# Kernel optimization log

Measured on AMD Instinct MI355X. Metric: run time of the kernel, lower is better.

Reference implementation:

```python
import jax, jax.numpy as jnp
import numpy as np

K = 128
T_X = 4
DATA_LENGTH = 512
B_GROUPS = 64
B = B_GROUPS * DATA_LENGTH
INV_SQRT2 = 0.7071067811865476  # 1/sqrt(2), haar reconstruction filter coeff


def setup_inputs() -> dict:
    key = jax.random.key(0)
    ks = jax.random.split(key, 9)
    x = jax.random.normal(ks[0], (B, T_X, K), jnp.float32)
    y = jax.random.normal(ks[1], (B, 1, K), jnp.float32)
    s = 1.0 / np.sqrt(K).astype(np.float32)
    Wq = jax.random.normal(ks[2], (K, K), jnp.float32) * s
    Wk = jax.random.normal(ks[3], (K, K), jnp.float32) * s
    Wv = jax.random.normal(ks[4], (K, K), jnp.float32) * s
    conv_w = jax.random.normal(ks[5], (K, 2 * K), jnp.float32) * (1.0 / np.sqrt(2 * K).astype(np.float32))
    conv_b = jax.random.normal(ks[6], (K,), jnp.float32) * 0.01
    bn_gamma = jnp.ones((K,), jnp.float32)
    bn_beta = jnp.zeros((K,), jnp.float32)
    bn_mean = jax.random.normal(ks[7], (K,), jnp.float32) * 0.1
    bn_var = jax.random.uniform(ks[8], (K,), jnp.float32, 0.5, 1.5)
    return dict(x=x, y=y, Wq=Wq, Wk=Wk, Wv=Wv, conv_w=conv_w, conv_b=conv_b,
                bn_gamma=bn_gamma, bn_beta=bn_beta, bn_mean=bn_mean, bn_var=bn_var,
                data_length=DATA_LENGTH)


def _idwt_haar(L, H):
    # inverse 1D haar transform along last dim: (Bg, C, 1, T) -> (Bg, C, 1, 2T)
    even = (L + H) * INV_SQRT2
    odd = (L - H) * INV_SQRT2
    out = jnp.stack([even, odd], axis=-1)  # (..., T, 2)
    return out.reshape(L.shape[:-1] + (L.shape[-1] * 2,))


def reference(x, y, Wq, Wk, Wv, conv_w, conv_b, bn_gamma, bn_beta, bn_mean, bn_var, data_length):
    b, t_x, k = x.shape  # t_x = 4 bands, heads = 1, t_y = 1
    q = jnp.einsum('btk,ok->bto', y, Wq)                      # (b, 1, k)
    keys = jnp.einsum('bsk,ok->bso', x, Wk) * (1.0 / (k ** 0.5))  # (b, 4, k)
    v = jnp.einsum('bsk,ok->bso', x, Wv)                      # (b, 4, k)
    dot = jnp.einsum('bto,bso->bs', q, keys)                  # (b, 4)
    w = jax.nn.softmax(dot, axis=1)                           # softmax over the 4 bands
    outs = w[:, :, None] * v                                  # (b, 4, k) band-weighted values
    Bg = b // data_length
    # per band: (b, k) -> (Bg, dl, 1, k) -> permute -> (Bg, k, 1, dl)
    o = outs.reshape(Bg, data_length, t_x, k).transpose(2, 0, 3, 1)  # (4, Bg, k, dl)
    o = o[:, :, :, None, :]                                   # (4, Bg, k, 1, dl)
    out_L = _idwt_haar(o[0], o[1])                            # (Bg, k, 1, 2*dl)
    out_H = _idwt_haar(o[2], o[3])
    out = jnp.concatenate([out_L, out_H], axis=1)             # (Bg, 2k, 1, 2*dl)
    # transition: 1x1 conv + BN (eval mode) + LeakyReLU(0.01)
    z = jnp.einsum('bcij,oc->boij', out, conv_w) + conv_b[None, :, None, None]
    scale = (bn_gamma * jax.lax.rsqrt(bn_var + 1e-5))[None, :, None, None]
    z = (z - bn_mean[None, :, None, None]) * scale + bn_beta[None, :, None, None]
    return jnp.where(z > 0, z, 0.01 * z)
```

## Files before the change

### kernel.cpp

```cpp
#include <hip/hip_runtime.h>
#include <stdint.h>

typedef __attribute__((ext_vector_type(8))) short bf16x8;
typedef __attribute__((ext_vector_type(4))) float f32x4;

__device__ __forceinline__ unsigned short f2bf(float x) {
    union { float f; uint32_t u; } v; v.f = x;
    uint32_t r = v.u + 0x7FFFu + ((v.u >> 16) & 1u);
    return (unsigned short)(r >> 16);
}
__device__ __forceinline__ uint32_t pack2bf(float a, float b) {
    return (uint32_t)f2bf(a) | ((uint32_t)f2bf(b) << 16);
}
__device__ __forceinline__ float bf2f(uint32_t lo) {
    union { uint32_t u; float f; } v; v.u = lo << 16; return v.f;
}
__device__ __forceinline__ float lrelu(float v) { return v > 0.f ? v : 0.01f * v; }

__global__ __launch_bounds__(256) void precompute_kernel(
    const float* __restrict__ Wq, const float* __restrict__ Wk,
    const float* __restrict__ Wv, const float* __restrict__ conv_w,
    const float* __restrict__ conv_b, const float* __restrict__ bn_gamma,
    const float* __restrict__ bn_beta, const float* __restrict__ bn_mean,
    const float* __restrict__ bn_var,
    unsigned short* __restrict__ Gh, unsigned short* __restrict__ Gl,
    unsigned short* __restrict__ Mh,
    float* __restrict__ scale2, float* __restrict__ bias2)
{
    __shared__ float lds0[2176];
    __shared__ float lds1[2176];
    const int tid = threadIdx.x;
    const int bid = blockIdx.x;

    if (bid == 192) {
        if (tid < 128) {
            float sc = bn_gamma[tid] * rsqrtf(bn_var[tid] + 1e-5f);
            scale2[tid] = sc;
            bias2[tid]  = (conv_b[tid] - bn_mean[tid]) * sc + bn_beta[tid];
        }
        return;
    }

    if (bid < 64) {
        int i0 = (bid >> 3) << 4, j0 = (bid & 7) << 4;
        #pragma unroll
        for (int t = 0; t < 8; ++t) {
            int e = tid + t * 256;
            int o = e >> 4, c = e & 15;
            lds0[o * 17 + c] = Wk[o * 128 + i0 + c];
            lds1[o * 17 + c] = Wq[o * 128 + j0 + c];
        }
        __syncthreads();
        int ti = tid >> 4, tj = tid & 15;
        float sum = 0.f;
        #pragma unroll 8
        for (int o = 0; o < 128; ++o) sum += lds0[o * 17 + ti] * lds1[o * 17 + tj];
        float val = sum * 0.08838834764831845f;
        unsigned short h = f2bf(val);
        int idx = (i0 + ti) * 128 + j0 + tj;
        Gh[idx] = h;
        Gl[idx] = f2bf(val - bf2f(h));
    } else {
        int rel = bid - 64;
        int o0 = (rel >> 4) << 4, c0 = (rel & 15) << 4;
        int cw0 = (c0 >> 7) << 7, cc0 = c0 & 127;
        #pragma unroll
        for (int t = 0; t < 8; ++t) {
            int e = tid + t * 256;
            int to = e >> 7, k = e & 127;
            lds0[to * 132 + k] = conv_w[(o0 + to) * 256 + cw0 + k];
            int kk = e >> 4, c = e & 15;
            lds1[kk * 17 + c] = Wv[kk * 128 + cc0 + c];
        }
        __syncthreads();
        int to = tid >> 4, tc = tid & 15;
        float sum = 0.f;
        #pragma unroll 8
        for (int k = 0; k < 128; ++k) sum += lds0[to * 132 + k] * lds1[k * 17 + tc];
        Mh[(o0 + to) * 256 + c0 + tc] = f2bf(sum * 0.7071067811865476f);
    }
}

#define AADDR(row, gi)   (((row) << 8) + ((((gi) ^ ((row) & 7))) << 4))

__global__ __launch_bounds__(256, 4) void fused_kernel(
    const float* __restrict__ x, const float* __restrict__ y,
    const unsigned short* __restrict__ Gh, const unsigned short* __restrict__ Gl,
    const unsigned short* __restrict__ Mh,
    const float* __restrict__ scale2, const float* __restrict__ bias2,
    float* __restrict__ out)
{
    __shared__ __align__(16) unsigned char smem[32768];
    float* gbufF = (float*)(smem + 16384);

    const int tid = threadIdx.x;
    const int w = tid >> 6;
    const int l = tid & 63;
    const int quad = l >> 4;
    const int i16 = l & 15;
    const int bid = blockIdx.x;
    const int b0 = bid * 32;

    union F8 { float4 v[2]; float f[8]; };
    F8 X[2][4];
    #pragma unroll
    for (int pass = 0; pass < 2; ++pass) {
        int b_loc = 8 * w + pass * 4 + quad;
        const float* xb = x + (size_t)(b0 + b_loc) * 512 + i16 * 8;
        #pragma unroll
        for (int t = 0; t < 4; ++t) {
            X[pass][t].v[0] = *(const float4*)(xb + t * 128);
            X[pass][t].v[1] = *(const float4*)(xb + t * 128 + 4);
        }
    }
    const int ks0 = bid & 3;
    bf16x8 pgh[2], pgl[2];
    #pragma unroll
    for (int n = 0; n < 2; ++n) {
        int off = ((2 * w + n) * 16 + i16) * 128 + ks0 * 32 + quad * 8;
        pgh[n] = *(const bf16x8*)(Gh + off);
        pgl[n] = *(const bf16x8*)(Gl + off);
    }

    {
        const float* yb = y + (size_t)b0 * 128;
        #pragma unroll
        for (int it = 0; it < 2; ++it) {
            int j = tid + it * 256;
            int row = j >> 4, gk = j & 15;
            float4 v0 = *(const float4*)(yb + row * 128 + gk * 8);
            float4 v1 = *(const float4*)(yb + row * 128 + gk * 8 + 4);
            float f[8] = {v0.x, v0.y, v0.z, v0.w, v1.x, v1.y, v1.z, v1.w};
            uint32_t hi[4], lo[4];
            #pragma unroll
            for (int e = 0; e < 4; ++e) {
                unsigned short h0 = f2bf(f[2 * e]), h1 = f2bf(f[2 * e + 1]);
                hi[e] = (uint32_t)h0 | ((uint32_t)h1 << 16);
                lo[e] = (uint32_t)f2bf(f[2 * e] - bf2f(h0)) |
                        ((uint32_t)f2bf(f[2 * e + 1] - bf2f(h1)) << 16);
            }
            int addr = AADDR(row, gk);
            *(uint4*)(smem + addr)        = make_uint4(hi[0], hi[1], hi[2], hi[3]);
            *(uint4*)(smem + 8192 + addr) = make_uint4(lo[0], lo[1], lo[2], lo[3]);
        }
    }
    __syncthreads();

    {
        f32x4 accg[2][2];
        #pragma unroll
        for (int rt = 0; rt < 2; ++rt)
            #pragma unroll
            for (int n = 0; n < 2; ++n) accg[rt][n] = (f32x4){0.f, 0.f, 0.f, 0.f};
        #pragma unroll
        for (int ks = 0; ks < 4; ++ks) {
            int ksr = (ks + bid) & 3;
            bf16x8 ah[2], al[2];
            #pragma unroll
            for (int rt = 0; rt < 2; ++rt) {
                int row = 16 * rt + i16;
                int addr = AADDR(row, ksr * 4 + quad);
                ah[rt] = *(const bf16x8*)(smem + addr);
                al[rt] = *(const bf16x8*)(smem + 8192 + addr);
            }
            #pragma unroll
            for (int n = 0; n < 2; ++n) {
                bf16x8 bh, bl;
                if (ks == 0) { bh = pgh[n]; bl = pgl[n]; }
                else {
                    int off = ((2 * w + n) * 16 + i16) * 128 + ksr * 32 + quad * 8;
                    bh = *(const bf16x8*)(Gh + off);
                    bl = *(const bf16x8*)(Gl + off);
                }
                #pragma unroll
                for (int rt = 0; rt < 2; ++rt) {
                    accg[rt][n] = __builtin_amdgcn_mfma_f32_16x16x32_bf16(ah[rt], bh, accg[rt][n], 0, 0, 0);
                    accg[rt][n] = __builtin_amdgcn_mfma_f32_16x16x32_bf16(al[rt], bh, accg[rt][n], 0, 0, 0);
                    accg[rt][n] = __builtin_amdgcn_mfma_f32_16x16x32_bf16(ah[rt], bl, accg[rt][n], 0, 0, 0);
                }
            }
        }
        #pragma unroll
        for (int n = 0; n < 2; ++n) {
            int i = (2 * w + n) * 16 + i16;
            #pragma unroll
            for (int rt = 0; rt < 2; ++rt)
                #pragma unroll
                for (int r = 0; r < 4; ++r)
                    gbufF[(16 * rt + quad * 4 + r) * 128 + i] = accg[rt][n][r];
        }
    }
    __syncthreads();

    #pragma unroll
    for (int pass = 0; pass < 2; ++pass) {
        int b_loc = 8 * w + pass * 4 + quad;
        float4 ga = *(const float4*)(gbufF + b_loc * 128 + i16 * 8);
        float4 gb = *(const float4*)(gbufF + b_loc * 128 + i16 * 8 + 4);
        float p[4];
        #pragma unroll
        for (int t = 0; t < 4; ++t) {
            float4 a = X[pass][t].v[0], b = X[pass][t].v[1];
            p[t] = a.x * ga.x + a.y * ga.y + a.z * ga.z + a.w * ga.w
                 + b.x * gb.x + b.y * gb.y + b.z * gb.z + b.w * gb.w;
        }
        #pragma unroll
        for (int off = 8; off >= 1; off >>= 1) {
            p[0] += __shfl_xor(p[0], off);
            p[1] += __shfl_xor(p[1], off);
            p[2] += __shfl_xor(p[2], off);
            p[3] += __shfl_xor(p[3], off);
        }
        float mx = fmaxf(fmaxf(p[0], p[1]), fmaxf(p[2], p[3]));
        float e0 = __expf(p[0] - mx), e1 = __expf(p[1] - mx);
        float e2 = __expf(p[2] - mx), e3 = __expf(p[3] - mx);
        float inv = 1.f / (e0 + e1 + e2 + e3);
        float w0 = e0 * inv, w1 = e1 * inv, w2 = e2 * inv, w3 = e3 * inv;
        int r0 = 2 * b_loc, r1 = r0 + 1;
        int a0 = AADDR(r0, i16), a1 = AADDR(r1, i16);
        uint32_t eL[4], oL[4], eH[4], oH[4];
        #pragma unroll
        for (int e = 0; e < 4; ++e) {
            int c0 = 2 * e, c1 = 2 * e + 1;
            eL[e] = pack2bf(w0 * X[pass][0].f[c0] + w1 * X[pass][1].f[c0], w0 * X[pass][0].f[c1] + w1 * X[pass][1].f[c1]);
            oL[e] = pack2bf(w0 * X[pass][0].f[c0] - w1 * X[pass][1].f[c0], w0 * X[pass][0].f[c1] - w1 * X[pass][1].f[c1]);
            eH[e] = pack2bf(w2 * X[pass][2].f[c0] + w3 * X[pass][3].f[c0], w2 * X[pass][2].f[c1] + w3 * X[pass][3].f[c1]);
            oH[e] = pack2bf(w2 * X[pass][2].f[c0] - w3 * X[pass][3].f[c0], w2 * X[pass][2].f[c1] - w3 * X[pass][3].f[c1]);
        }
        *(uint4*)(smem + a0)         = make_uint4(eL[0], eL[1], eL[2], eL[3]);
        *(uint4*)(smem + a1)         = make_uint4(oL[0], oL[1], oL[2], oL[3]);
        *(uint4*)(smem + 16384 + a0) = make_uint4(eH[0], eH[1], eH[2], eH[3]);
        *(uint4*)(smem + 16384 + a1) = make_uint4(oH[0], oH[1], oH[2], oH[3]);
    }

    const int ks0b = bid & 7;
    bf16x8 pmh[2];
    {
        int half = ks0b >> 2, kk = ks0b & 3;
        #pragma unroll
        for (int n = 0; n < 2; ++n)
            pmh[n] = *(const bf16x8*)(Mh + ((2 * w + n) * 16 + i16) * 256 + half * 128 + kk * 32 + quad * 8);
    }
    __syncthreads();

    f32x4 acc[4][2];
    #pragma unroll
    for (int rb = 0; rb < 4; ++rb)
        #pragma unroll
        for (int n = 0; n < 2; ++n) acc[rb][n] = (f32x4){0.f, 0.f, 0.f, 0.f};

    #pragma unroll
    for (int ks = 0; ks < 8; ++ks) {
        int ksr = (ks + bid) & 7;
        int half = ksr >> 2, kk = ksr & 3;
        int base = half << 14;
        int gi = kk * 4 + quad;
        bf16x8 a[4];
        #pragma unroll
        for (int rb = 0; rb < 4; ++rb)
            a[rb] = *(const bf16x8*)(smem + base + AADDR(16 * rb + i16, gi));
        #pragma unroll
        for (int n = 0; n < 2; ++n) {
            bf16x8 bh;
            if (ks == 0) bh = pmh[n];
            else bh = *(const bf16x8*)(Mh + ((2 * w + n) * 16 + i16) * 256 + half * 128 + kk * 32 + quad * 8);
            #pragma unroll
            for (int rb = 0; rb < 4; ++rb)
                acc[rb][n] = __builtin_amdgcn_mfma_f32_16x16x32_bf16(a[rb], bh, acc[rb][n], 0, 0, 0);
        }
    }

    {
        float* outp = out + (size_t)(bid >> 4) * 131072 + (bid & 15) * 64;
        #pragma unroll
        for (int n = 0; n < 2; ++n) {
            int o = (2 * w + n) * 16 + i16;
            float sc = scale2[o], bi = bias2[o];
            #pragma unroll
            for (int rb = 0; rb < 4; ++rb) {
                int jb = 16 * rb + quad * 4;
                f32x4 a = acc[rb][n];
                float4 r;
                r.x = lrelu(a[0] * sc + bi);
                r.y = lrelu(a[1] * sc + bi);
                r.z = lrelu(a[2] * sc + bi);
                r.w = lrelu(a[3] * sc + bi);
                *(float4*)(outp + (size_t)o * 1024 + jb) = r;
            }
        }
    }
}

extern "C" void kernel_launch(void* const* d_in, const int* in_sizes, int n_in,
                              void* d_out, int out_size, void* d_ws, size_t ws_size,
                              hipStream_t stream)
{
    (void)in_sizes; (void)n_in; (void)out_size; (void)ws_size;
    const float* x        = (const float*)d_in[0];
    const float* y        = (const float*)d_in[1];
    const float* Wq       = (const float*)d_in[2];
    const float* Wk       = (const float*)d_in[3];
    const float* Wv       = (const float*)d_in[4];
    const float* conv_w   = (const float*)d_in[5];
    const float* conv_b   = (const float*)d_in[6];
    const float* bn_gamma = (const float*)d_in[7];
    const float* bn_beta  = (const float*)d_in[8];
    const float* bn_mean  = (const float*)d_in[9];
    const float* bn_var   = (const float*)d_in[10];

    unsigned char* ws = (unsigned char*)d_ws;
    unsigned short* Gh = (unsigned short*)(ws);
    unsigned short* Gl = (unsigned short*)(ws + 32768);
    unsigned short* Mh = (unsigned short*)(ws + 65536);
    float* scale2      = (float*)(ws + 131072);
    float* bias2       = (float*)(ws + 131584);

    hipLaunchKernelGGL(precompute_kernel, dim3(193), dim3(256), 0, stream,
                       Wq, Wk, Wv, conv_w, conv_b, bn_gamma, bn_beta, bn_mean,
                       bn_var, Gh, Gl, Mh, scale2, bias2);
    hipLaunchKernelGGL(fused_kernel, dim3(1024), dim3(256), 0, stream,
                       x, y, Gh, Gl, Mh, scale2, bias2, (float*)d_out);
}
```

Before: 147.6 us.

## Halve rows per block and double grid to raise occupancy

Each block now handles 16 batch rows instead of 32. Shared memory drops to 16KB, the grid doubles to 2048 blocks, and launch bounds ask for 8 blocks per CU, all to hide memory latency through higher occupancy. The prefetch of the first G/M weight fragments is removed. The cost is twice as many reloads of the Gh/Gl/Mh weights per output row and smaller MFMA tiles with less register reuse. The output writes become 32-float segments per row instead of 64, which is less contiguous.

```diff
diff --git a/kernel.cpp b/kernel.cpp
--- a/kernel.cpp
+++ b/kernel.cpp
@@ -83,15 +83,15 @@
 
 #define AADDR(row, gi)   (((row) << 8) + ((((gi) ^ ((row) & 7))) << 4))
 
-__global__ __launch_bounds__(256, 4) void fused_kernel(
+__global__ __launch_bounds__(256, 8) void fused_kernel(
     const float* __restrict__ x, const float* __restrict__ y,
     const unsigned short* __restrict__ Gh, const unsigned short* __restrict__ Gl,
     const unsigned short* __restrict__ Mh,
     const float* __restrict__ scale2, const float* __restrict__ bias2,
     float* __restrict__ out)
 {
-    __shared__ __align__(16) unsigned char smem[32768];
-    float* gbufF = (float*)(smem + 16384);
+    __shared__ __align__(16) unsigned char smem[16384];
+    float* gbufF = (float*)(smem + 8192);
 
     const int tid = threadIdx.x;
     const int w = tid >> 6;
@@ -99,108 +99,77 @@
     const int quad = l >> 4;
     const int i16 = l & 15;
     const int bid = blockIdx.x;
-    const int b0 = bid * 32;
+    const int b0 = bid * 16;
+    const int b_loc = 4 * w + quad;
 
     union F8 { float4 v[2]; float f[8]; };
-    F8 X[2][4];
-    #pragma unroll
-    for (int pass = 0; pass < 2; ++pass) {
-        int b_loc = 8 * w + pass * 4 + quad;
+    F8 X[4];
+    {
         const float* xb = x + (size_t)(b0 + b_loc) * 512 + i16 * 8;
         #pragma unroll
         for (int t = 0; t < 4; ++t) {
-            X[pass][t].v[0] = *(const float4*)(xb + t * 128);
-            X[pass][t].v[1] = *(const float4*)(xb + t * 128 + 4);
-        }
-    }
-    const int ks0 = bid & 3;
-    bf16x8 pgh[2], pgl[2];
-    #pragma unroll
-    for (int n = 0; n < 2; ++n) {
-        int off = ((2 * w + n) * 16 + i16) * 128 + ks0 * 32 + quad * 8;
-        pgh[n] = *(const bf16x8*)(Gh + off);
-        pgl[n] = *(const bf16x8*)(Gl + off);
-    }
-
-    {
-        const float* yb = y + (size_t)b0 * 128;
-        #pragma unroll
-        for (int it = 0; it < 2; ++it) {
-            int j = tid + it * 256;
-            int row = j >> 4, gk = j & 15;
-            float4 v0 = *(const float4*)(yb + row * 128 + gk * 8);
-            float4 v1 = *(const float4*)(yb + row * 128 + gk * 8 + 4);
-            float f[8] = {v0.x, v0.y, v0.z, v0.w, v1.x, v1.y, v1.z, v1.w};
-            uint32_t hi[4], lo[4];
-            #pragma unroll
-            for (int e = 0; e < 4; ++e) {
-                unsigned short h0 = f2bf(f[2 * e]), h1 = f2bf(f[2 * e + 1]);
-                hi[e] = (uint32_t)h0 | ((uint32_t)h1 << 16);
-                lo[e] = (uint32_t)f2bf(f[2 * e] - bf2f(h0)) |
-                        ((uint32_t)f2bf(f[2 * e + 1] - bf2f(h1)) << 16);
-            }
-            int addr = AADDR(row, gk);
-            *(uint4*)(smem + addr)        = make_uint4(hi[0], hi[1], hi[2], hi[3]);
-            *(uint4*)(smem + 8192 + addr) = make_uint4(lo[0], lo[1], lo[2], lo[3]);
-        }
+            X[t].v[0] = *(const float4*)(xb + t * 128);
+            X[t].v[1] = *(const float4*)(xb + t * 128 + 4);
+        }
+    }
+
+    {
+        int row = tid >> 4, gk = tid & 15;
+        const float* yb = y + (size_t)(b0 + row) * 128 + gk * 8;
+        float4 v0 = *(const float4*)(yb);
+        float4 v1 = *(const float4*)(yb + 4);
+        float f[8] = {v0.x, v0.y, v0.z, v0.w, v1.x, v1.y, v1.z, v1.w};
+        uint32_t hi[4], lo[4];
+        #pragma unroll
+        for (int e = 0; e < 4; ++e) {
+            unsigned short h0 = f2bf(f[2 * e]), h1 = f2bf(f[2 * e + 1]);
+            hi[e] = (uint32_t)h0 | ((uint32_t)h1 << 16);
+            lo[e] = (uint32_t)f2bf(f[2 * e] - bf2f(h0)) |
+                    ((uint32_t)f2bf(f[2 * e + 1] - bf2f(h1)) << 16);
+        }
+        int addr = AADDR(row, gk);
+        *(uint4*)(smem + addr)        = make_uint4(hi[0], hi[1], hi[2], hi[3]);
+        *(uint4*)(smem + 4096 + addr) = make_uint4(lo[0], lo[1], lo[2], lo[3]);
     }
     __syncthreads();
 
     {
-        f32x4 accg[2][2];
-        #pragma unroll
-        for (int rt = 0; rt < 2; ++rt)
-            #pragma unroll
-            for (int n = 0; n < 2; ++n) accg[rt][n] = (f32x4){0.f, 0.f, 0.f, 0.f};
+        f32x4 accg[2];
+        accg[0] = (f32x4){0.f, 0.f, 0.f, 0.f};
+        accg[1] = (f32x4){0.f, 0.f, 0.f, 0.f};
         #pragma unroll
         for (int ks = 0; ks < 4; ++ks) {
             int ksr = (ks + bid) & 3;
-            bf16x8 ah[2], al[2];
-            #pragma unroll
-            for (int rt = 0; rt < 2; ++rt) {
-                int row = 16 * rt + i16;
-                int addr = AADDR(row, ksr * 4 + quad);
-                ah[rt] = *(const bf16x8*)(smem + addr);
-                al[rt] = *(const bf16x8*)(smem + 8192 + addr);
-            }
+            int aaddr = AADDR(i16, ksr * 4 + quad);
+            bf16x8 ah = *(const bf16x8*)(smem + aaddr);
+            bf16x8 al = *(const bf16x8*)(smem + 4096 + aaddr);
             #pragma unroll
             for (int n = 0; n < 2; ++n) {
-                bf16x8 bh, bl;
-                if (ks == 0) { bh = pgh[n]; bl = pgl[n]; }
-                else {
-                    int off = ((2 * w + n) * 16 + i16) * 128 + ksr * 32 + quad * 8;
-                    bh = *(const bf16x8*)(Gh + off);
-                    bl = *(const bf16x8*)(Gl + off);
-                }
-                #pragma unroll
-                for (int rt = 0; rt < 2; ++rt) {
-                    accg[rt][n] = __builtin_amdgcn_mfma_f32_16x16x32_bf16(ah[rt], bh, accg[rt][n], 0, 0, 0);
-                    accg[rt][n] = __builtin_amdgcn_mfma_f32_16x16x32_bf16(al[rt], bh, accg[rt][n], 0, 0, 0);
-                    accg[rt][n] = __builtin_amdgcn_mfma_f32_16x16x32_bf16(ah[rt], bl, accg[rt][n], 0, 0, 0);
-                }
+                int off = ((2 * w + n) * 16 + i16) * 128 + ksr * 32 + quad * 8;
+                bf16x8 bh = *(const bf16x8*)(Gh + off);
+                bf16x8 bl = *(const bf16x8*)(Gl + off);
+                accg[n] = __builtin_amdgcn_mfma_f32_16x16x32_bf16(ah, bh, accg[n], 0, 0, 0);
+                accg[n] = __builtin_amdgcn_mfma_f32_16x16x32_bf16(al, bh, accg[n], 0, 0, 0);
+                accg[n] = __builtin_amdgcn_mfma_f32_16x16x32_bf16(ah, bl, accg[n], 0, 0, 0);
             }
         }
         #pragma unroll
         for (int n = 0; n < 2; ++n) {
             int i = (2 * w + n) * 16 + i16;
             #pragma unroll
-            for (int rt = 0; rt < 2; ++rt)
-                #pragma unroll
-                for (int r = 0; r < 4; ++r)
-                    gbufF[(16 * rt + quad * 4 + r) * 128 + i] = accg[rt][n][r];
+            for (int r = 0; r < 4; ++r)
+                gbufF[(quad * 4 + r) * 128 + i] = accg[n][r];
         }
     }
     __syncthreads();
 
-    #pragma unroll
-    for (int pass = 0; pass < 2; ++pass) {
-        int b_loc = 8 * w + pass * 4 + quad;
+    {
         float4 ga = *(const float4*)(gbufF + b_loc * 128 + i16 * 8);
         float4 gb = *(const float4*)(gbufF + b_loc * 128 + i16 * 8 + 4);
         float p[4];
         #pragma unroll
         for (int t = 0; t < 4; ++t) {
-            float4 a = X[pass][t].v[0], b = X[pass][t].v[1];
+            float4 a = X[t].v[0], b = X[t].v[1];
             p[t] = a.x * ga.x + a.y * ga.y + a.z * ga.z + a.w * ga.w
                  + b.x * gb.x + b.y * gb.y + b.z * gb.z + b.w * gb.w;
         }
@@ -216,36 +185,27 @@
         float e2 = __expf(p[2] - mx), e3 = __expf(p[3] - mx);
         float inv = 1.f / (e0 + e1 + e2 + e3);
         float w0 = e0 * inv, w1 = e1 * inv, w2 = e2 * inv, w3 = e3 * inv;
-        int r0 = 2 * b_loc, r1 = r0 + 1;
-        int a0 = AADDR(r0, i16), a1 = AADDR(r1, i16);
+        int r0 = 2 * b_loc;
+        int a0 = AADDR(r0, i16), a1 = AADDR(r0 + 1, i16);
         uint32_t eL[4], oL[4], eH[4], oH[4];
         #pragma unroll
         for (int e = 0; e < 4; ++e) {
             int c0 = 2 * e, c1 = 2 * e + 1;
-            eL[e] = pack2bf(w0 * X[pass][0].f[c0] + w1 * X[pass][1].f[c0], w0 * X[pass][0].f[c1] + w1 * X[pass][1].f[c1]);
-            oL[e] = pack2bf(w0 * X[pass][0].f[c0] - w1 * X[pass][1].f[c0], w0 * X[pass][0].f[c1] - w1 * X[pass][1].f[c1]);
-            eH[e] = pack2bf(w2 * X[pass][2].f[c0] + w3 * X[pass][3].f[c0], w2 * X[pass][2].f[c1] + w3 * X[pass][3].f[c1]);
-            oH[e] = pack2bf(w2 * X[pass][2].f[c0] - w3 * X[pass][3].f[c0], w2 * X[pass][2].f[c1] - w3 * X[pass][3].f[c1]);
-        }
-        *(uint4*)(smem + a0)         = make_uint4(eL[0], eL[1], eL[2], eL[3]);
-        *(uint4*)(smem + a1)         = make_uint4(oL[0], oL[1], oL[2], oL[3]);
-        *(uint4*)(smem + 16384 + a0) = make_uint4(eH[0], eH[1], eH[2], eH[3]);
-        *(uint4*)(smem + 16384 + a1) = make_uint4(oH[0], oH[1], oH[2], oH[3]);
-    }
-
-    const int ks0b = bid & 7;
-    bf16x8 pmh[2];
-    {
-        int half = ks0b >> 2, kk = ks0b & 3;
-        #pragma unroll
-        for (int n = 0; n < 2; ++n)
-            pmh[n] = *(const bf16x8*)(Mh + ((2 * w + n) * 16 + i16) * 256 + half * 128 + kk * 32 + quad * 8);
+            eL[e] = pack2bf(w0 * X[0].f[c0] + w1 * X[1].f[c0], w0 * X[0].f[c1] + w1 * X[1].f[c1]);
+            oL[e] = pack2bf(w0 * X[0].f[c0] - w1 * X[1].f[c0], w0 * X[0].f[c1] - w1 * X[1].f[c1]);
+            eH[e] = pack2bf(w2 * X[2].f[c0] + w3 * X[3].f[c0], w2 * X[2].f[c1] + w3 * X[3].f[c1]);
+            oH[e] = pack2bf(w2 * X[2].f[c0] - w3 * X[3].f[c0], w2 * X[2].f[c1] - w3 * X[3].f[c1]);
+        }
+        *(uint4*)(smem + a0)        = make_uint4(eL[0], eL[1], eL[2], eL[3]);
+        *(uint4*)(smem + a1)        = make_uint4(oL[0], oL[1], oL[2], oL[3]);
+        *(uint4*)(smem + 8192 + a0) = make_uint4(eH[0], eH[1], eH[2], eH[3]);
+        *(uint4*)(smem + 8192 + a1) = make_uint4(oH[0], oH[1], oH[2], oH[3]);
     }
     __syncthreads();
 
-    f32x4 acc[4][2];
+    f32x4 acc[2][2];
     #pragma unroll
-    for (int rb = 0; rb < 4; ++rb)
+    for (int rb = 0; rb < 2; ++rb)
         #pragma unroll
         for (int n = 0; n < 2; ++n) acc[rb][n] = (f32x4){0.f, 0.f, 0.f, 0.f};
 
@@ -253,31 +213,26 @@
     for (int ks = 0; ks < 8; ++ks) {
         int ksr = (ks + bid) & 7;
         int half = ksr >> 2, kk = ksr & 3;
-        int base = half << 14;
+        int base = half << 13;
         int gi = kk * 4 + quad;
-        bf16x8 a[4];
-        #pragma unroll
-        for (int rb = 0; rb < 4; ++rb)
-            a[rb] = *(const bf16x8*)(smem + base + AADDR(16 * rb + i16, gi));
+        bf16x8 a0v = *(const bf16x8*)(smem + base + AADDR(i16, gi));
+        bf16x8 a1v = *(const bf16x8*)(smem + base + AADDR(16 + i16, gi));
         #pragma unroll
         for (int n = 0; n < 2; ++n) {
-            bf16x8 bh;
-            if (ks == 0) bh = pmh[n];
-            else bh = *(const bf16x8*)(Mh + ((2 * w + n) * 16 + i16) * 256 + half * 128 + kk * 32 + quad * 8);
-            #pragma unroll
-            for (int rb = 0; rb < 4; ++rb)
-                acc[rb][n] = __builtin_amdgcn_mfma_f32_16x16x32_bf16(a[rb], bh, acc[rb][n], 0, 0, 0);
-        }
-    }
-
-    {
-        float* outp = out + (size_t)(bid >> 4) * 131072 + (bid & 15) * 64;
+            bf16x8 bh = *(const bf16x8*)(Mh + ((2 * w + n) * 16 + i16) * 256 + half * 128 + kk * 32 + quad * 8);
+            acc[0][n] = __builtin_amdgcn_mfma_f32_16x16x32_bf16(a0v, bh, acc[0][n], 0, 0, 0);
+            acc[1][n] = __builtin_amdgcn_mfma_f32_16x16x32_bf16(a1v, bh, acc[1][n], 0, 0, 0);
+        }
+    }
+
+    {
+        float* outp = out + (size_t)(bid >> 5) * 131072 + (bid & 31) * 32;
         #pragma unroll
         for (int n = 0; n < 2; ++n) {
             int o = (2 * w + n) * 16 + i16;
             float sc = scale2[o], bi = bias2[o];
             #pragma unroll
-            for (int rb = 0; rb < 4; ++rb) {
+            for (int rb = 0; rb < 2; ++rb) {
                 int jb = 16 * rb + quad * 4;
                 f32x4 a = acc[rb][n];
                 float4 r;
@@ -318,6 +273,6 @@
     hipLaunchKernelGGL(precompute_kernel, dim3(193), dim3(256), 0, stream,
                        Wq, Wk, Wv, conv_w, conv_b, bn_gamma, bn_beta, bn_mean,
                        bn_var, Gh, Gl, Mh, scale2, bias2);
-    hipLaunchKernelGGL(fused_kernel, dim3(1024), dim3(256), 0, stream,
+    hipLaunchKernelGGL(fused_kernel, dim3(2048), dim3(256), 0, stream,
                        x, y, Gh, Gl, Mh, scale2, bias2, (float*)d_out);
 }
```

Result: slower. 170.7 us (+15.7%).

## Split fused kernel into separate g-projection and softmax/conv kernels via workspace

Applied to the files above, without the earlier changes.

Splits the single fused kernel into two: one computes g = y·(Wq^T Wk) with split-bf16 MFMA and writes it to a 16 MB workspace buffer, and a second reads g and x, does the softmax, Haar mixing and 1x1 conv GEMM. The aim is to lower register and LDS pressure in the main kernel (it now pins 4 waves per EU) and shorten its critical path. The cost is an extra launch plus a round trip of the g tensor through global memory. It falls back to the old fused kernel when the workspace is too small.

```diff
diff --git a/kernel.cpp b/kernel.cpp
--- a/kernel.cpp
+++ b/kernel.cpp
@@ -83,6 +83,237 @@
 
 #define AADDR(row, gi)   (((row) << 8) + ((((gi) ^ ((row) & 7))) << 4))
 
+__global__ __launch_bounds__(256) void g_kernel(
+    const float* __restrict__ y,
+    const unsigned short* __restrict__ Gh, const unsigned short* __restrict__ Gl,
+    float* __restrict__ g)
+{
+    __shared__ __align__(16) unsigned char smem[16384];
+    const int tid = threadIdx.x;
+    const int w = tid >> 6;
+    const int l = tid & 63;
+    const int quad = l >> 4;
+    const int i16 = l & 15;
+    const int bid = blockIdx.x;
+    const int b0 = bid * 32;
+
+    float4 yv[2][2];
+    int rowA[2], gkA[2];
+    #pragma unroll
+    for (int it = 0; it < 2; ++it) {
+        int j = tid + it * 256;
+        rowA[it] = j >> 4; gkA[it] = j & 15;
+        const float* yb = y + (size_t)(b0 + rowA[it]) * 128 + gkA[it] * 8;
+        yv[it][0] = *(const float4*)(yb);
+        yv[it][1] = *(const float4*)(yb + 4);
+    }
+    const int ks0 = bid & 3;
+    bf16x8 pgh[2], pgl[2];
+    #pragma unroll
+    for (int n = 0; n < 2; ++n) {
+        int off = ((2 * w + n) * 16 + i16) * 128 + ks0 * 32 + quad * 8;
+        pgh[n] = *(const bf16x8*)(Gh + off);
+        pgl[n] = *(const bf16x8*)(Gl + off);
+    }
+
+    #pragma unroll
+    for (int it = 0; it < 2; ++it) {
+        float f[8] = {yv[it][0].x, yv[it][0].y, yv[it][0].z, yv[it][0].w,
+                      yv[it][1].x, yv[it][1].y, yv[it][1].z, yv[it][1].w};
+        uint32_t hi[4], lo[4];
+        #pragma unroll
+        for (int e = 0; e < 4; ++e) {
+            unsigned short h0 = f2bf(f[2 * e]), h1 = f2bf(f[2 * e + 1]);
+            hi[e] = (uint32_t)h0 | ((uint32_t)h1 << 16);
+            lo[e] = (uint32_t)f2bf(f[2 * e] - bf2f(h0)) |
+                    ((uint32_t)f2bf(f[2 * e + 1] - bf2f(h1)) << 16);
+        }
+        int addr = AADDR(rowA[it], gkA[it]);
+        *(uint4*)(smem + addr)        = make_uint4(hi[0], hi[1], hi[2], hi[3]);
+        *(uint4*)(smem + 8192 + addr) = make_uint4(lo[0], lo[1], lo[2], lo[3]);
+    }
+    __syncthreads();
+
+    f32x4 accg[2][2];
+    #pragma unroll
+    for (int rt = 0; rt < 2; ++rt)
+        #pragma unroll
+        for (int n = 0; n < 2; ++n) accg[rt][n] = (f32x4){0.f, 0.f, 0.f, 0.f};
+    #pragma unroll
+    for (int ks = 0; ks < 4; ++ks) {
+        int ksr = (ks + bid) & 3;
+        bf16x8 ah[2], al[2];
+        #pragma unroll
+        for (int rt = 0; rt < 2; ++rt) {
+            int row = 16 * rt + i16;
+            int addr = AADDR(row, ksr * 4 + quad);
+            ah[rt] = *(const bf16x8*)(smem + addr);
+            al[rt] = *(const bf16x8*)(smem + 8192 + addr);
+        }
+        #pragma unroll
+        for (int n = 0; n < 2; ++n) {
+            bf16x8 bh, bl;
+            if (ks == 0) { bh = pgh[n]; bl = pgl[n]; }
+            else {
+                int off = ((2 * w + n) * 16 + i16) * 128 + ksr * 32 + quad * 8;
+                bh = *(const bf16x8*)(Gh + off);
+                bl = *(const bf16x8*)(Gl + off);
+            }
+            #pragma unroll
+            for (int rt = 0; rt < 2; ++rt) {
+                accg[rt][n] = __builtin_amdgcn_mfma_f32_16x16x32_bf16(ah[rt], bh, accg[rt][n], 0, 0, 0);
+                accg[rt][n] = __builtin_amdgcn_mfma_f32_16x16x32_bf16(al[rt], bh, accg[rt][n], 0, 0, 0);
+                accg[rt][n] = __builtin_amdgcn_mfma_f32_16x16x32_bf16(ah[rt], bl, accg[rt][n], 0, 0, 0);
+            }
+        }
+    }
+    #pragma unroll
+    for (int n = 0; n < 2; ++n) {
+        int i = (2 * w + n) * 16 + i16;
+        #pragma unroll
+        for (int rt = 0; rt < 2; ++rt)
+            #pragma unroll
+            for (int r = 0; r < 4; ++r)
+                g[(size_t)(b0 + 16 * rt + quad * 4 + r) * 128 + i] = accg[rt][n][r];
+    }
+}
+
+__global__ __launch_bounds__(256)
+__attribute__((amdgpu_waves_per_eu(4, 4)))
+void fused2_kernel(
+    const float* __restrict__ x, const float* __restrict__ g,
+    const unsigned short* __restrict__ Mh,
+    const float* __restrict__ scale2, const float* __restrict__ bias2,
+    float* __restrict__ out)
+{
+    __shared__ __align__(16) unsigned char smem[32768];
+    const int tid = threadIdx.x;
+    const int w = tid >> 6;
+    const int l = tid & 63;
+    const int quad = l >> 4;
+    const int i16 = l & 15;
+    const int bid = blockIdx.x;
+    const int b0 = bid * 32;
+
+    union F8 { float4 v[2]; float f[8]; };
+    F8 Gv[2];
+    #pragma unroll
+    for (int pass = 0; pass < 2; ++pass) {
+        int b_loc = 8 * w + pass * 4 + quad;
+        const float* gp = g + (size_t)(b0 + b_loc) * 128 + i16 * 8;
+        Gv[pass].v[0] = *(const float4*)(gp);
+        Gv[pass].v[1] = *(const float4*)(gp + 4);
+    }
+    F8 X[2][4];
+    #pragma unroll
+    for (int pass = 0; pass < 2; ++pass) {
+        int b_loc = 8 * w + pass * 4 + quad;
+        const float* xb = x + (size_t)(b0 + b_loc) * 512 + i16 * 8;
+        #pragma unroll
+        for (int t = 0; t < 4; ++t) {
+            X[pass][t].v[0] = *(const float4*)(xb + t * 128);
+            X[pass][t].v[1] = *(const float4*)(xb + t * 128 + 4);
+        }
+    }
+
+    #pragma unroll
+    for (int pass = 0; pass < 2; ++pass) {
+        int b_loc = 8 * w + pass * 4 + quad;
+        float4 ga = Gv[pass].v[0], gb = Gv[pass].v[1];
+        float p[4];
+        #pragma unroll
+        for (int t = 0; t < 4; ++t) {
+            float4 a = X[pass][t].v[0], b = X[pass][t].v[1];
+            p[t] = a.x * ga.x + a.y * ga.y + a.z * ga.z + a.w * ga.w
+                 + b.x * gb.x + b.y * gb.y + b.z * gb.z + b.w * gb.w;
+        }
+        #pragma unroll
+        for (int off = 8; off >= 1; off >>= 1) {
+            p[0] += __shfl_xor(p[0], off);
+            p[1] += __shfl_xor(p[1], off);
+            p[2] += __shfl_xor(p[2], off);
+            p[3] += __shfl_xor(p[3], off);
+        }
+        float mx = fmaxf(fmaxf(p[0], p[1]), fmaxf(p[2], p[3]));
+        float e0 = __expf(p[0] - mx), e1 = __expf(p[1] - mx);
+        float e2 = __expf(p[2] - mx), e3 = __expf(p[3] - mx);
+        float inv = 1.f / (e0 + e1 + e2 + e3);
+        float w0 = e0 * inv, w1 = e1 * inv, w2 = e2 * inv, w3 = e3 * inv;
+        int r0 = 2 * b_loc, r1 = r0 + 1;
+        int a0 = AADDR(r0, i16), a1 = AADDR(r1, i16);
+        uint32_t eL[4], oL[4], eH[4], oH[4];
+        #pragma unroll
+        for (int e = 0; e < 4; ++e) {
+            int c0 = 2 * e, c1 = 2 * e + 1;
+            eL[e] = pack2bf(w0 * X[pass][0].f[c0] + w1 * X[pass][1].f[c0], w0 * X[pass][0].f[c1] + w1 * X[pass][1].f[c1]);
+            oL[e] = pack2bf(w0 * X[pass][0].f[c0] - w1 * X[pass][1].f[c0], w0 * X[pass][0].f[c1] - w1 * X[pass][1].f[c1]);
+            eH[e] = pack2bf(w2 * X[pass][2].f[c0] + w3 * X[pass][3].f[c0], w2 * X[pass][2].f[c1] + w3 * X[pass][3].f[c1]);
+            oH[e] = pack2bf(w2 * X[pass][2].f[c0] - w3 * X[pass][3].f[c0], w2 * X[pass][2].f[c1] - w3 * X[pass][3].f[c1]);
+        }
+        *(uint4*)(smem + a0)         = make_uint4(eL[0], eL[1], eL[2], eL[3]);
+        *(uint4*)(smem + a1)         = make_uint4(oL[0], oL[1], oL[2], oL[3]);
+        *(uint4*)(smem + 16384 + a0) = make_uint4(eH[0], eH[1], eH[2], eH[3]);
+        *(uint4*)(smem + 16384 + a1) = make_uint4(oH[0], oH[1], oH[2], oH[3]);
+    }
+
+    const int ks0b = bid & 7;
+    bf16x8 pmh[2];
+    {
+        int half = ks0b >> 2, kk = ks0b & 3;
+        #pragma unroll
+        for (int n = 0; n < 2; ++n)
+            pmh[n] = *(const bf16x8*)(Mh + ((2 * w + n) * 16 + i16) * 256 + half * 128 + kk * 32 + quad * 8);
+    }
+    __syncthreads();
+
+    f32x4 acc[4][2];
+    #pragma unroll
+    for (int rb = 0; rb < 4; ++rb)
+        #pragma unroll
+        for (int n = 0; n < 2; ++n) acc[rb][n] = (f32x4){0.f, 0.f, 0.f, 0.f};
+
+    #pragma unroll
+    for (int ks = 0; ks < 8; ++ks) {
+        int ksr = (ks + bid) & 7;
+        int half = ksr >> 2, kk = ksr & 3;
+        int base = half << 14;
+        int gi = kk * 4 + quad;
+        bf16x8 a[4];
+        #pragma unroll
+        for (int rb = 0; rb < 4; ++rb)
+            a[rb] = *(const bf16x8*)(smem + base + AADDR(16 * rb + i16, gi));
+        #pragma unroll
+        for (int n = 0; n < 2; ++n) {
+            bf16x8 bh;
+            if (ks == 0) bh = pmh[n];
+            else bh = *(const bf16x8*)(Mh + ((2 * w + n) * 16 + i16) * 256 + half * 128 + kk * 32 + quad * 8);
+            #pragma unroll
+            for (int rb = 0; rb < 4; ++rb)
+                acc[rb][n] = __builtin_amdgcn_mfma_f32_16x16x32_bf16(a[rb], bh, acc[rb][n], 0, 0, 0);
+        }
+    }
+
+    {
+        float* outp = out + (size_t)(bid >> 4) * 131072 + (bid & 15) * 64;
+        #pragma unroll
+        for (int n = 0; n < 2; ++n) {
+            int o = (2 * w + n) * 16 + i16;
+            float sc = scale2[o], bi = bias2[o];
+            #pragma unroll
+            for (int rb = 0; rb < 4; ++rb) {
+                int jb = 16 * rb + quad * 4;
+                f32x4 a = acc[rb][n];
+                float4 r;
+                r.x = lrelu(a[0] * sc + bi);
+                r.y = lrelu(a[1] * sc + bi);
+                r.z = lrelu(a[2] * sc + bi);
+                r.w = lrelu(a[3] * sc + bi);
+                *(float4*)(outp + (size_t)o * 1024 + jb) = r;
+            }
+        }
+    }
+}
+
 __global__ __launch_bounds__(256, 4) void fused_kernel(
     const float* __restrict__ x, const float* __restrict__ y,
     const unsigned short* __restrict__ Gh, const unsigned short* __restrict__ Gl,
@@ -295,7 +526,7 @@
                               void* d_out, int out_size, void* d_ws, size_t ws_size,
                               hipStream_t stream)
 {
-    (void)in_sizes; (void)n_in; (void)out_size; (void)ws_size;
+    (void)in_sizes; (void)n_in; (void)out_size;
     const float* x        = (const float*)d_in[0];
     const float* y        = (const float*)d_in[1];
     const float* Wq       = (const float*)d_in[2];
@@ -314,10 +545,20 @@
     unsigned short* Mh = (unsigned short*)(ws + 65536);
     float* scale2      = (float*)(ws + 131072);
     float* bias2       = (float*)(ws + 131584);
+    const size_t G_OFF = 135168;
+    float* gbuf        = (float*)(ws + G_OFF);
+    const size_t need  = G_OFF + (size_t)32768 * 128 * 4;
 
     hipLaunchKernelGGL(precompute_kernel, dim3(193), dim3(256), 0, stream,
                        Wq, Wk, Wv, conv_w, conv_b, bn_gamma, bn_beta, bn_mean,
                        bn_var, Gh, Gl, Mh, scale2, bias2);
-    hipLaunchKernelGGL(fused_kernel, dim3(1024), dim3(256), 0, stream,
-                       x, y, Gh, Gl, Mh, scale2, bias2, (float*)d_out);
-}
+    if (ws_size >= need) {
+        hipLaunchKernelGGL(g_kernel, dim3(1024), dim3(256), 0, stream,
+                           y, Gh, Gl, gbuf);
+        hipLaunchKernelGGL(fused2_kernel, dim3(1024), dim3(256), 0, stream,
+                           x, gbuf, Mh, scale2, bias2, (float*)d_out);
+    } else {
+        hipLaunchKernelGGL(fused_kernel, dim3(1024), dim3(256), 0, stream,
+                           x, y, Gh, Gl, Mh, scale2, bias2, (float*)d_out);
+    }
+}
```

New measurement: 156.3 us. 5.9% more time.
